# Performance work log

Measured on AMD Instinct MI355X. Metric: run time of the kernel, lower is better.

Reference implementation:

```python
import jax, jax.numpy as jnp
import numpy as np

N_NODES = 100000
N_EDGES = 1600000
N_PAIRS = 200000
IN_C, HID_C, OUT_C = 128, 128, 64


def setup_inputs() -> dict:
    key = jax.random.key(0)
    ks = jax.random.split(key, 10)
    x = jax.random.normal(ks[0], (N_NODES, IN_C), dtype=jnp.float32)
    edge_index = jax.random.randint(ks[1], (2, N_EDGES), 0, N_NODES, dtype=jnp.int64)
    node_i = jax.random.randint(ks[2], (N_PAIRS,), 0, N_NODES, dtype=jnp.int64)
    node_j = jax.random.randint(ks[3], (N_PAIRS,), 0, N_NODES, dtype=jnp.int64)
    def glorot(k, fan_in, fan_out):
        s = jnp.sqrt(6.0 / (fan_in + fan_out))
        return jax.random.uniform(k, (fan_in, fan_out), jnp.float32, -s, s)
    W1 = glorot(ks[4], IN_C, HID_C)
    b1 = jnp.zeros((HID_C,), jnp.float32)
    W2 = glorot(ks[5], HID_C, HID_C)
    b2 = jnp.zeros((HID_C,), jnp.float32)
    W3 = glorot(ks[6], HID_C, OUT_C)
    b3 = jnp.zeros((OUT_C,), jnp.float32)
    return {"x": x, "edge_index": edge_index, "node_i": node_i, "node_j": node_j,
            "W1": W1, "b1": b1, "W2": W2, "b2": b2, "W3": W3, "b3": b3}


def _gcn_layer(h, src, dst, deg_inv, w_e, W, b):
    # h: [N, Cin] -> linear then symmetric-normalized aggregation (with self loops)
    h = h @ W  # [N, Cout]
    msg = h[src] * w_e[:, None]  # [E, Cout] gather + edge weight
    agg = jax.ops.segment_sum(msg, dst, num_segments=N_NODES)
    agg = agg + h * deg_inv[:, None]  # self-loop term: h_i / deg_i
    return agg + b


def reference(x, edge_index, node_i, node_j, W1, b1, W2, b2, W3, b3):
    src, dst = edge_index[0], edge_index[1]
    # GCN normalization with self loops: deg_i = 1 + in-degree
    ones = jnp.ones((N_EDGES,), jnp.float32)
    deg = jax.ops.segment_sum(ones, dst, num_segments=N_NODES) + 1.0
    dinv_sqrt = jax.lax.rsqrt(deg)
    deg_inv = 1.0 / deg
    w_e = dinv_sqrt[src] * dinv_sqrt[dst]  # [E]

    h = _gcn_layer(x, src, dst, deg_inv, w_e, W1, b1)
    h = jax.nn.relu(h)  # dropout is identity in eval mode
    h = _gcn_layer(h, src, dst, deg_inv, w_e, W2, b2)
    h = jax.nn.relu(h)
    h = _gcn_layer(h, src, dst, deg_inv, w_e, W3, b3)

    # dot-product link decode (decode_type=None)
    return jnp.sum(h[node_i] * h[node_j], axis=-1)  # [N_PAIRS]
```

## Files before the change

kernel.cpp:

```cpp
#include <hip/hip_runtime.h>

#define NN 100000
#define NNP 100032
#define NE 1600000
#define NP 200000
#define NBKT 782
#define BCAP 3072
#define BKB 4096

typedef short s16x8 __attribute__((ext_vector_type(8)));
typedef float f32x4 __attribute__((ext_vector_type(4)));

__device__ __forceinline__ unsigned short f2bf(float f) {
  unsigned int u = __float_as_uint(f);
  u += 0x7fffu + ((u >> 16) & 1u);
  return (unsigned short)(u >> 16);
}

__device__ __forceinline__ void upadd(uint u, float& lo, float& hi) {
  lo += __uint_as_float(u << 16);
  hi += __uint_as_float(u & 0xffff0000u);
}

template <int NT>
__device__ __forceinline__ void prepw_dev(const float* __restrict__ W,
                                          uint* __restrict__ Wt, int tid) {
  constexpr int COUT = NT * 16;
  if (tid >= 4 * NT * 64) return;
  int lane = tid & 63, comb = tid >> 6;
  int ks = comb / NT, tl = comb % NT;
  int q = lane >> 4, n = lane & 15;
  uint w[4];
#pragma unroll
  for (int jj = 0; jj < 4; ++jj) {
    int k0 = ks * 32 + q * 8 + 2 * jj;
    uint lo = f2bf(W[k0 * COUT + tl * 16 + n]);
    uint hi = f2bf(W[(k0 + 1) * COUT + tl * 16 + n]);
    w[jj] = lo | (hi << 16);
  }
  ((uint4*)Wt)[comb * 64 + lane] = make_uint4(w[0], w[1], w[2], w[3]);
}

__global__ __launch_bounds__(256) void k_setup(const float* __restrict__ W1,
                                               const float* __restrict__ W2,
                                               const float* __restrict__ W3,
                                               uint* __restrict__ Wt1,
                                               uint* __restrict__ Wt2,
                                               uint* __restrict__ Wt3,
                                               int* __restrict__ gcur) {
  int b = blockIdx.x, t = threadIdx.x;
  if (b < 4) {
    int i = b * 256 + t;
    if (i < 1024) gcur[i] = i * BCAP;
  } else if (b < 12) {
    prepw_dev<8>(W1, Wt1, (b - 4) * 256 + t);
  } else if (b < 20) {
    prepw_dev<8>(W2, Wt2, (b - 12) * 256 + t);
  } else {
    prepw_dev<4>(W3, Wt3, (b - 20) * 256 + t);
  }
}

__global__ __launch_bounds__(256) void k_bucket(const int* __restrict__ ei,
                                                int* __restrict__ gcur,
                                                int* __restrict__ aux) {
  __shared__ int cnt[1024];
  __shared__ int scn[1024];
  __shared__ int cur[1024];
  __shared__ int sc[256];
  __shared__ int sorted[BKB];
  __shared__ unsigned short sbkt[BKB];
  const int t = threadIdx.x;
  const int base = blockIdx.x * BKB;

  for (int i = t; i < 1024; i += 256) cnt[i] = 0;
  __syncthreads();

  int pk[16], bk[16];
#pragma unroll
  for (int i = 0; i < 16; ++i) {
    int e = base + t + 256 * i;
    if (e < NE) {
      int src = ei[e], dst = ei[NE + e];
      bk[i] = dst >> 7;
      pk[i] = src | ((dst & 127) << 17);
      atomicAdd(&cnt[bk[i]], 1);
    } else {
      bk[i] = -1;
    }
  }
  __syncthreads();

  int s0 = cnt[4 * t], s1 = cnt[4 * t + 1], s2 = cnt[4 * t + 2], s3 = cnt[4 * t + 3];
  int local = s0 + s1 + s2 + s3;
  sc[t] = local;
  __syncthreads();
  for (int off = 1; off < 256; off <<= 1) {
    int a = (t >= off) ? sc[t - off] : 0;
    __syncthreads();
    sc[t] += a;
    __syncthreads();
  }
  int b0 = sc[t] - local;
  scn[4 * t] = b0;
  scn[4 * t + 1] = b0 + s0;
  scn[4 * t + 2] = b0 + s0 + s1;
  scn[4 * t + 3] = b0 + s0 + s1 + s2;
  cur[4 * t] = scn[4 * t];
  cur[4 * t + 1] = scn[4 * t + 1];
  cur[4 * t + 2] = scn[4 * t + 2];
  cur[4 * t + 3] = scn[4 * t + 3];
  __syncthreads();
  const int tot = sc[255];

#pragma unroll
  for (int i = 0; i < 16; ++i) {
    if (bk[i] >= 0) {
      int pos = atomicAdd(&cur[bk[i]], 1);
      sorted[pos] = pk[i];
      sbkt[pos] = (unsigned short)bk[i];
    }
  }
  __syncthreads();

  for (int b = t; b < 1024; b += 256) {
    int c = cnt[b];
    if (c > 0) cur[b] = atomicAdd(&gcur[b], c);
  }
  __syncthreads();

  for (int k = t; k < tot; k += 256) {
    int b = sbkt[k];
    aux[cur[b] + (k - scn[b])] = sorted[k];
  }
}

__global__ __launch_bounds__(256) void k_csr(const int* __restrict__ gcur,
                                             const int* __restrict__ aux,
                                             int* __restrict__ row_ptr,
                                             float* __restrict__ dinv,
                                             int* __restrict__ col) {
  __shared__ int red[256];
  __shared__ int c[128];
  __shared__ int cur[128];
  const int b = blockIdx.x, t = threadIdx.x;
  int p = 0;
  for (int i = t; i < b; i += 256) p += gcur[i] - i * BCAP;
  red[t] = p;
  if (t < 128) c[t] = 0;
  __syncthreads();
  for (int off = 128; off > 0; off >>= 1) {
    if (t < off) red[t] += red[t + off];
    __syncthreads();
  }
  const int base = red[0];
  const int m = gcur[b] - b * BCAP;
  const int* a = aux + (size_t)b * BCAP;
  __syncthreads();
  for (int k = t; k < m; k += 256) atomicAdd(&c[a[k] >> 17], 1);
  __syncthreads();
  int val = (t < 128) ? c[t] : 0;
  red[t] = val;
  __syncthreads();
  for (int off = 1; off < 128; off <<= 1) {
    int add = (t >= off && t < 128) ? red[t - off] : 0;
    __syncthreads();
    if (t < 128) red[t] += add;
    __syncthreads();
  }
  if (t < 128) {
    int excl = red[t] - val + base;
    int node = b * 128 + t;
    if (node < NN) {
      row_ptr[node] = excl;
      dinv[node] = rsqrtf((float)(val + 1));
      cur[t] = excl;
    }
  }
  if (b == NBKT - 1 && t == 0) row_ptr[NN] = base + m;
  __syncthreads();
  for (int k = t; k < m; k += 256) {
    int pk2 = a[k];
    int pos = atomicAdd(&cur[pk2 >> 17], 1);
    col[pos] = pk2 & 0x1FFFF;
  }
}

template <int COUT, bool AFP32>
__global__ __launch_bounds__(256) void k_gemm_mfma(const void* __restrict__ Av,
                                                   const uint* __restrict__ Wt,
                                                   const float* __restrict__ dinv,
                                                   unsigned short* __restrict__ T) {
  constexpr int NT = COUT / 16;
  __shared__ __align__(16) uint Wlds[4 * NT * 64 * 4];
  __shared__ __align__(16) unsigned short Obuf[64 * COUT];
  const int t = threadIdx.x;
  {
    const uint4* src = (const uint4*)Wt;
    uint4* dst = (uint4*)Wlds;
    for (int i = t; i < 4 * NT * 64; i += 256) dst[i] = src[i];
  }
  __syncthreads();

  const int wv = t >> 6, lane = t & 63;
  const int n = lane & 15, quad = lane >> 4;
  const int rbase = blockIdx.x * 64 + wv * 16;

  union AB { uint4 u; s16x8 s; };
  AB a[4];
  if constexpr (AFP32) {
    const float* A = (const float*)Av;
    int row = rbase + n;
    if (row >= NN) row = NN - 1;
    const float* ap = A + (size_t)row * 128;
#pragma unroll
    for (int ks = 0; ks < 4; ++ks) {
      float4 v0 = *(const float4*)(ap + ks * 32 + quad * 8);
      float4 v1 = *(const float4*)(ap + ks * 32 + quad * 8 + 4);
      a[ks].u.x = (uint)f2bf(v0.x) | ((uint)f2bf(v0.y) << 16);
      a[ks].u.y = (uint)f2bf(v0.z) | ((uint)f2bf(v0.w) << 16);
      a[ks].u.z = (uint)f2bf(v1.x) | ((uint)f2bf(v1.y) << 16);
      a[ks].u.w = (uint)f2bf(v1.z) | ((uint)f2bf(v1.w) << 16);
    }
  } else {
    const uint4* A = (const uint4*)Av;
    int row = rbase + n;
#pragma unroll
    for (int ks = 0; ks < 4; ++ks) a[ks].u = A[(size_t)row * 16 + ks * 4 + quad];
  }

  f32x4 acc[NT];
#pragma unroll
  for (int tl = 0; tl < NT; ++tl) acc[tl] = (f32x4){0.f, 0.f, 0.f, 0.f};

#pragma unroll
  for (int ks = 0; ks < 4; ++ks) {
#pragma unroll
    for (int tl = 0; tl < NT; ++tl) {
      AB b;
      b.u = *(const uint4*)&Wlds[((ks * NT + tl) * 64 + lane) * 4];
      acc[tl] = __builtin_amdgcn_mfma_f32_16x16x32_bf16(a[ks].s, b.s, acc[tl], 0, 0, 0);
    }
  }

  float4 dv = *(const float4*)(dinv + rbase + quad * 4);
  float dvv[4] = {dv.x, dv.y, dv.z, dv.w};
  unsigned short* ob = Obuf + wv * 16 * COUT;
#pragma unroll
  for (int tl = 0; tl < NT; ++tl)
#pragma unroll
    for (int r = 0; r < 4; ++r)
      ob[(quad * 4 + r) * COUT + tl * 16 + n] = f2bf(acc[tl][r] * dvv[r]);

  uint4* gdst = (uint4*)(T + (size_t)rbase * COUT);
  constexpr int ITER = COUT / 32;
#pragma unroll
  for (int i = 0; i < ITER; ++i) {
    int off16 = i * 64 + lane;
    int lrow = (off16 * 8) / COUT;
    uint4 v = make_uint4(0u, 0u, 0u, 0u);
    if (rbase + lrow < NN) v = *(const uint4*)&ob[off16 * 8];
    gdst[off16] = v;
  }
}

__global__ __launch_bounds__(256) void k_gather12(const int* __restrict__ row_ptr,
                                                  const int* __restrict__ col,
                                                  const uint4* __restrict__ T4,
                                                  const float* __restrict__ dinv,
                                                  const float* __restrict__ bias,
                                                  uint4* __restrict__ An) {
  int w = (blockIdx.x * 256 + threadIdx.x) >> 6;
  int lane = threadIdx.x & 63;
  if (w >= NN) return;
  int s = row_ptr[w], tend = row_ptr[w + 1];
  const int q = lane >> 4;
  const int cl = lane & 15;
  float acc[8] = {0.f, 0.f, 0.f, 0.f, 0.f, 0.f, 0.f, 0.f};
  if (q == 0) {
    uint4 u = T4[(size_t)w * 16 + cl];
    upadd(u.x, acc[0], acc[1]);
    upadd(u.y, acc[2], acc[3]);
    upadd(u.z, acc[4], acc[5]);
    upadd(u.w, acc[6], acc[7]);
  }
  const int iters = (tend - s + 15) >> 4;
  const int m = tend - 1;
  int e = s + q;
  for (int it = 0; it < iters; ++it, e += 16) {
    int i0 = e, i1 = e + 4, i2 = e + 8, i3 = e + 12;
    int c0 = col[min(i0, m)], c1 = col[min(i1, m)];
    int c2 = col[min(i2, m)], c3 = col[min(i3, m)];
    c0 = (i0 < tend) ? c0 : NN;
    c1 = (i1 < tend) ? c1 : NN;
    c2 = (i2 < tend) ? c2 : NN;
    c3 = (i3 < tend) ? c3 : NN;
    uint4 v0 = T4[(size_t)c0 * 16 + cl];
    uint4 v1 = T4[(size_t)c1 * 16 + cl];
    uint4 v2 = T4[(size_t)c2 * 16 + cl];
    uint4 v3 = T4[(size_t)c3 * 16 + cl];
    upadd(v0.x, acc[0], acc[1]); upadd(v0.y, acc[2], acc[3]);
    upadd(v0.z, acc[4], acc[5]); upadd(v0.w, acc[6], acc[7]);
    upadd(v1.x, acc[0], acc[1]); upadd(v1.y, acc[2], acc[3]);
    upadd(v1.z, acc[4], acc[5]); upadd(v1.w, acc[6], acc[7]);
    upadd(v2.x, acc[0], acc[1]); upadd(v2.y, acc[2], acc[3]);
    upadd(v2.z, acc[4], acc[5]); upadd(v2.w, acc[6], acc[7]);
    upadd(v3.x, acc[0], acc[1]); upadd(v3.y, acc[2], acc[3]);
    upadd(v3.z, acc[4], acc[5]); upadd(v3.w, acc[6], acc[7]);
  }
#pragma unroll
  for (int i = 0; i < 8; ++i) {
    acc[i] += __shfl_down(acc[i], 16, 64);
    acc[i] += __shfl_down(acc[i], 32, 64);
  }
  if (q == 0) {
    float4 b0 = *(const float4*)&bias[cl * 8];
    float4 b1 = *(const float4*)&bias[cl * 8 + 4];
    float dv = dinv[w];
    float r[8];
    r[0] = fmaxf(fmaf(dv, acc[0], b0.x), 0.f);
    r[1] = fmaxf(fmaf(dv, acc[1], b0.y), 0.f);
    r[2] = fmaxf(fmaf(dv, acc[2], b0.z), 0.f);
    r[3] = fmaxf(fmaf(dv, acc[3], b0.w), 0.f);
    r[4] = fmaxf(fmaf(dv, acc[4], b1.x), 0.f);
    r[5] = fmaxf(fmaf(dv, acc[5], b1.y), 0.f);
    r[6] = fmaxf(fmaf(dv, acc[6], b1.z), 0.f);
    r[7] = fmaxf(fmaf(dv, acc[7], b1.w), 0.f);
    uint4 o;
    o.x = (uint)f2bf(r[0]) | ((uint)f2bf(r[1]) << 16);
    o.y = (uint)f2bf(r[2]) | ((uint)f2bf(r[3]) << 16);
    o.z = (uint)f2bf(r[4]) | ((uint)f2bf(r[5]) << 16);
    o.w = (uint)f2bf(r[6]) | ((uint)f2bf(r[7]) << 16);
    An[(size_t)w * 16 + cl] = o;
  }
}

__global__ __launch_bounds__(256) void k_gather3(const int* __restrict__ row_ptr,
                                                 const int* __restrict__ col,
                                                 const uint4* __restrict__ T4,
                                                 float* __restrict__ G3) {
  int w = (blockIdx.x * 256 + threadIdx.x) >> 6;
  int lane = threadIdx.x & 63;
  if (w >= NN) return;
  int s = row_ptr[w], tend = row_ptr[w + 1];
  const int g = lane >> 3;
  const int cl = lane & 7;
  float acc[8] = {0.f, 0.f, 0.f, 0.f, 0.f, 0.f, 0.f, 0.f};
  if (g == 0) {
    uint4 u = T4[(size_t)w * 8 + cl];
    upadd(u.x, acc[0], acc[1]);
    upadd(u.y, acc[2], acc[3]);
    upadd(u.z, acc[4], acc[5]);
    upadd(u.w, acc[6], acc[7]);
  }
  const int iters = (tend - s + 15) >> 4;
  const int m = tend - 1;
  int e = s + g;
  for (int it = 0; it < iters; ++it, e += 16) {
    int i0 = e, i1 = e + 8;
    int c0 = col[min(i0, m)], c1 = col[min(i1, m)];
    c0 = (i0 < tend) ? c0 : NN;
    c1 = (i1 < tend) ? c1 : NN;
    uint4 v0 = T4[(size_t)c0 * 8 + cl];
    uint4 v1 = T4[(size_t)c1 * 8 + cl];
    upadd(v0.x, acc[0], acc[1]); upadd(v0.y, acc[2], acc[3]);
    upadd(v0.z, acc[4], acc[5]); upadd(v0.w, acc[6], acc[7]);
    upadd(v1.x, acc[0], acc[1]); upadd(v1.y, acc[2], acc[3]);
    upadd(v1.z, acc[4], acc[5]); upadd(v1.w, acc[6], acc[7]);
  }
#pragma unroll
  for (int i = 0; i < 8; ++i) {
    acc[i] += __shfl_down(acc[i], 8, 64);
    acc[i] += __shfl_down(acc[i], 16, 64);
    acc[i] += __shfl_down(acc[i], 32, 64);
  }
  if (g == 0) {
    float* gp = &G3[(size_t)w * 64 + cl * 8];
    *(float4*)gp = make_float4(acc[0], acc[1], acc[2], acc[3]);
    *(float4*)(gp + 4) = make_float4(acc[4], acc[5], acc[6], acc[7]);
  }
}

__global__ __launch_bounds__(256) void k_decode(const int* __restrict__ ni,
                                                const int* __restrict__ nj,
                                                const float* __restrict__ G3,
                                                const float* __restrict__ dinv,
                                                const float* __restrict__ b3,
                                                float* __restrict__ out) {
  int p = blockIdx.x * 16 + (threadIdx.x >> 4);
  int cl = threadIdx.x & 15;
  int i = ni[p], j = nj[p];
  float4 gi = *(const float4*)&G3[(size_t)i * 64 + cl * 4];
  float4 gj = *(const float4*)&G3[(size_t)j * 64 + cl * 4];
  float4 bb = *(const float4*)&b3[cl * 4];
  float di = dinv[i], dj = dinv[j];
  float v = fmaf(di, gi.x, bb.x) * fmaf(dj, gj.x, bb.x) +
            fmaf(di, gi.y, bb.y) * fmaf(dj, gj.y, bb.y) +
            fmaf(di, gi.z, bb.z) * fmaf(dj, gj.z, bb.z) +
            fmaf(di, gi.w, bb.w) * fmaf(dj, gj.w, bb.w);
  v += __shfl_xor(v, 1, 64);
  v += __shfl_xor(v, 2, 64);
  v += __shfl_xor(v, 4, 64);
  v += __shfl_xor(v, 8, 64);
  if (cl == 0) out[p] = v;
}

extern "C" void kernel_launch(void* const* d_in, const int* in_sizes, int n_in,
                              void* d_out, int out_size, void* d_ws, size_t ws_size,
                              hipStream_t stream) {
  const float* x  = (const float*)d_in[0];
  const int*   ei = (const int*)d_in[1];
  const int*   ni = (const int*)d_in[2];
  const int*   nj = (const int*)d_in[3];
  const float* W1 = (const float*)d_in[4];
  const float* b1 = (const float*)d_in[5];
  const float* W2 = (const float*)d_in[6];
  const float* b2 = (const float*)d_in[7];
  const float* W3 = (const float*)d_in[8];
  const float* b3 = (const float*)d_in[9];
  float* out = (float*)d_out;

  float* dinv    = (float*)d_ws;
  int*   row_ptr = (int*)(dinv + 102400);
  int*   gcur    = row_ptr + 102400;
  int*   col     = gcur + 1024;
  uint*  Wt1     = (uint*)(col + NE);
  uint*  Wt2     = Wt1 + 8192;
  uint*  Wt3     = Wt2 + 8192;
  uint*  Tbf     = Wt3 + 4096;
  uint*  Abf     = Tbf + (size_t)NNP * 64;
  float* G3      = (float*)(Abf + (size_t)NNP * 64);
  int*   aux     = (int*)G3;

  k_setup<<<24, 256, 0, stream>>>(W1, W2, W3, Wt1, Wt2, Wt3, gcur);
  k_bucket<<<(NE + BKB - 1) / BKB, 256, 0, stream>>>(ei, gcur, aux);
  k_csr<<<NBKT, 256, 0, stream>>>(gcur, aux, row_ptr, dinv, col);

  const int GB = NNP / 64;
  const int GATB = (NN * 64 + 255) / 256;

  k_gemm_mfma<128, true><<<GB, 256, 0, stream>>>(x, Wt1, dinv, (unsigned short*)Tbf);
  k_gather12<<<GATB, 256, 0, stream>>>(row_ptr, col, (const uint4*)Tbf, dinv, b1, (uint4*)Abf);
  k_gemm_mfma<128, false><<<GB, 256, 0, stream>>>(Abf, Wt2, dinv, (unsigned short*)Tbf);
  k_gather12<<<GATB, 256, 0, stream>>>(row_ptr, col, (const uint4*)Tbf, dinv, b2, (uint4*)Abf);
  k_gemm_mfma<64, false><<<GB, 256, 0, stream>>>(Abf, Wt3, dinv, (unsigned short*)Tbf);
  k_gather3<<<GATB, 256, 0, stream>>>(row_ptr, col, (const uint4*)Tbf, G3);
  k_decode<<<NP / 16, 256, 0, stream>>>(ni, nj, G3, dinv, b3, out);
}
```

Measured before the change: 345.0 us.

## Split layer-1/2 neighbor gather across eight column slices per node

Rewrites the hidden-layer aggregation so that each node is handled by 8 wavefronts, each covering a 32-byte column slice, instead of one wavefront covering all 128 channels. Each lane now does narrower 8-byte loads, and 16 edge groups per wave process two edges per iteration. The aim is more parallelism and memory-level concurrency, plus a smaller per-block working set of the feature table. The cost is re-reading row_ptr/col 8 times, a longer shuffle reduction, and 8x more wavefronts.

```diff
diff --git a/kernel.cpp b/kernel.cpp
--- a/kernel.cpp
+++ b/kernel.cpp
@@ -266,72 +266,55 @@
 
 __global__ __launch_bounds__(256) void k_gather12(const int* __restrict__ row_ptr,
                                                   const int* __restrict__ col,
-                                                  const uint4* __restrict__ T4,
+                                                  const char* __restrict__ Tb,
                                                   const float* __restrict__ dinv,
                                                   const float* __restrict__ bias,
-                                                  uint4* __restrict__ An) {
-  int w = (blockIdx.x * 256 + threadIdx.x) >> 6;
-  int lane = threadIdx.x & 63;
-  if (w >= NN) return;
-  int s = row_ptr[w], tend = row_ptr[w + 1];
-  const int q = lane >> 4;
-  const int cl = lane & 15;
-  float acc[8] = {0.f, 0.f, 0.f, 0.f, 0.f, 0.f, 0.f, 0.f};
-  if (q == 0) {
-    uint4 u = T4[(size_t)w * 16 + cl];
-    upadd(u.x, acc[0], acc[1]);
-    upadd(u.y, acc[2], acc[3]);
-    upadd(u.z, acc[4], acc[5]);
-    upadd(u.w, acc[6], acc[7]);
-  }
-  const int iters = (tend - s + 15) >> 4;
+                                                  char* __restrict__ Anb) {
+  const int slice = blockIdx.x & 7;
+  const int node = (blockIdx.x >> 3) * 4 + (threadIdx.x >> 6);
+  const int lane = threadIdx.x & 63;
+  const int grp = lane >> 2, cl = lane & 3;
+  const uint soff = (uint)slice * 32 + (uint)cl * 8;
+  int s = row_ptr[node], tend = row_ptr[node + 1];
+  float a0 = 0.f, a1 = 0.f, a2 = 0.f, a3 = 0.f;
+  if (grp == 0) {
+    uint2 u = *(const uint2*)(Tb + (uint)node * 256 + soff);
+    upadd(u.x, a0, a1);
+    upadd(u.y, a2, a3);
+  }
+  const int iters = (tend - s + 31) >> 5;
   const int m = tend - 1;
-  int e = s + q;
-  for (int it = 0; it < iters; ++it, e += 16) {
-    int i0 = e, i1 = e + 4, i2 = e + 8, i3 = e + 12;
+  int e = s + grp;
+  for (int it = 0; it < iters; ++it, e += 32) {
+    int i0 = e, i1 = e + 16;
     int c0 = col[min(i0, m)], c1 = col[min(i1, m)];
-    int c2 = col[min(i2, m)], c3 = col[min(i3, m)];
     c0 = (i0 < tend) ? c0 : NN;
     c1 = (i1 < tend) ? c1 : NN;
-    c2 = (i2 < tend) ? c2 : NN;
-    c3 = (i3 < tend) ? c3 : NN;
-    uint4 v0 = T4[(size_t)c0 * 16 + cl];
-    uint4 v1 = T4[(size_t)c1 * 16 + cl];
-    uint4 v2 = T4[(size_t)c2 * 16 + cl];
-    uint4 v3 = T4[(size_t)c3 * 16 + cl];
-    upadd(v0.x, acc[0], acc[1]); upadd(v0.y, acc[2], acc[3]);
-    upadd(v0.z, acc[4], acc[5]); upadd(v0.w, acc[6], acc[7]);
-    upadd(v1.x, acc[0], acc[1]); upadd(v1.y, acc[2], acc[3]);
-    upadd(v1.z, acc[4], acc[5]); upadd(v1.w, acc[6], acc[7]);
-    upadd(v2.x, acc[0], acc[1]); upadd(v2.y, acc[2], acc[3]);
-    upadd(v2.z, acc[4], acc[5]); upadd(v2.w, acc[6], acc[7]);
-    upadd(v3.x, acc[0], acc[1]); upadd(v3.y, acc[2], acc[3]);
-    upadd(v3.z, acc[4], acc[5]); upadd(v3.w, acc[6], acc[7]);
-  }
-#pragma unroll
-  for (int i = 0; i < 8; ++i) {
-    acc[i] += __shfl_down(acc[i], 16, 64);
-    acc[i] += __shfl_down(acc[i], 32, 64);
-  }
-  if (q == 0) {
-    float4 b0 = *(const float4*)&bias[cl * 8];
-    float4 b1 = *(const float4*)&bias[cl * 8 + 4];
-    float dv = dinv[w];
-    float r[8];
-    r[0] = fmaxf(fmaf(dv, acc[0], b0.x), 0.f);
-    r[1] = fmaxf(fmaf(dv, acc[1], b0.y), 0.f);
-    r[2] = fmaxf(fmaf(dv, acc[2], b0.z), 0.f);
-    r[3] = fmaxf(fmaf(dv, acc[3], b0.w), 0.f);
-    r[4] = fmaxf(fmaf(dv, acc[4], b1.x), 0.f);
-    r[5] = fmaxf(fmaf(dv, acc[5], b1.y), 0.f);
-    r[6] = fmaxf(fmaf(dv, acc[6], b1.z), 0.f);
-    r[7] = fmaxf(fmaf(dv, acc[7], b1.w), 0.f);
-    uint4 o;
-    o.x = (uint)f2bf(r[0]) | ((uint)f2bf(r[1]) << 16);
-    o.y = (uint)f2bf(r[2]) | ((uint)f2bf(r[3]) << 16);
-    o.z = (uint)f2bf(r[4]) | ((uint)f2bf(r[5]) << 16);
-    o.w = (uint)f2bf(r[6]) | ((uint)f2bf(r[7]) << 16);
-    An[(size_t)w * 16 + cl] = o;
+    uint2 v0 = *(const uint2*)(Tb + (uint)c0 * 256 + soff);
+    uint2 v1 = *(const uint2*)(Tb + (uint)c1 * 256 + soff);
+    upadd(v0.x, a0, a1);
+    upadd(v0.y, a2, a3);
+    upadd(v1.x, a0, a1);
+    upadd(v1.y, a2, a3);
+  }
+#pragma unroll
+  for (int off = 4; off < 64; off <<= 1) {
+    a0 += __shfl_down(a0, off, 64);
+    a1 += __shfl_down(a1, off, 64);
+    a2 += __shfl_down(a2, off, 64);
+    a3 += __shfl_down(a3, off, 64);
+  }
+  if (lane < 4) {
+    float4 bb = *(const float4*)&bias[slice * 16 + cl * 4];
+    float dv = dinv[node];
+    float r0 = fmaxf(fmaf(dv, a0, bb.x), 0.f);
+    float r1 = fmaxf(fmaf(dv, a1, bb.y), 0.f);
+    float r2 = fmaxf(fmaf(dv, a2, bb.z), 0.f);
+    float r3 = fmaxf(fmaf(dv, a3, bb.w), 0.f);
+    uint2 o;
+    o.x = (uint)f2bf(r0) | ((uint)f2bf(r1) << 16);
+    o.y = (uint)f2bf(r2) | ((uint)f2bf(r3) << 16);
+    *(uint2*)(Anb + (uint)node * 256 + soff) = o;
   }
 }
 
@@ -437,12 +420,13 @@
   k_csr<<<NBKT, 256, 0, stream>>>(gcur, aux, row_ptr, dinv, col);
 
   const int GB = NNP / 64;
+  const int G12B = (NN / 4) * 8;
   const int GATB = (NN * 64 + 255) / 256;
 
   k_gemm_mfma<128, true><<<GB, 256, 0, stream>>>(x, Wt1, dinv, (unsigned short*)Tbf);
-  k_gather12<<<GATB, 256, 0, stream>>>(row_ptr, col, (const uint4*)Tbf, dinv, b1, (uint4*)Abf);
+  k_gather12<<<G12B, 256, 0, stream>>>(row_ptr, col, (const char*)Tbf, dinv, b1, (char*)Abf);
   k_gemm_mfma<128, false><<<GB, 256, 0, stream>>>(Abf, Wt2, dinv, (unsigned short*)Tbf);
-  k_gather12<<<GATB, 256, 0, stream>>>(row_ptr, col, (const uint4*)Tbf, dinv, b2, (uint4*)Abf);
+  k_gather12<<<G12B, 256, 0, stream>>>(row_ptr, col, (const char*)Tbf, dinv, b2, (char*)Abf);
   k_gemm_mfma<64, false><<<GB, 256, 0, stream>>>(Abf, Wt3, dinv, (unsigned short*)Tbf);
   k_gather3<<<GATB, 256, 0, stream>>>(row_ptr, col, (const uint4*)Tbf, G3);
   k_decode<<<NP / 16, 256, 0, stream>>>(ni, nj, G3, dinv, b3, out);
```

Result: slower. 695.7 us (+101.7%).

## Split layer-1/2 gather into two column halves with separate block ranges

Applied to the files above, without the earlier changes.

The 128-channel gather is split into two launches' worth of blocks, each handling 64 channels (128 bytes) of every node, with 8 lanes per half-row and 8 edge groups per wave. The first half of the grid processes channels 0-63 for all nodes and the second half processes channels 64-127. This shrinks the working set touched in the feature table at any one time so it fits the cache better. In exchange, the row_ptr and col indices are read twice and each thread keeps fewer loads in flight per iteration. Offsets now use 32-bit arithmetic.

```diff
diff --git a/kernel.cpp b/kernel.cpp
--- a/kernel.cpp
+++ b/kernel.cpp
@@ -7,6 +7,7 @@
 #define NBKT 782
 #define BCAP 3072
 #define BKB 4096
+#define G12H 25000
 
 typedef short s16x8 __attribute__((ext_vector_type(8)));
 typedef float f32x4 __attribute__((ext_vector_type(4)));
@@ -266,19 +267,20 @@
 
 __global__ __launch_bounds__(256) void k_gather12(const int* __restrict__ row_ptr,
                                                   const int* __restrict__ col,
-                                                  const uint4* __restrict__ T4,
+                                                  const char* __restrict__ Tb,
                                                   const float* __restrict__ dinv,
                                                   const float* __restrict__ bias,
-                                                  uint4* __restrict__ An) {
-  int w = (blockIdx.x * 256 + threadIdx.x) >> 6;
-  int lane = threadIdx.x & 63;
-  if (w >= NN) return;
-  int s = row_ptr[w], tend = row_ptr[w + 1];
-  const int q = lane >> 4;
-  const int cl = lane & 15;
+                                                  char* __restrict__ Anb) {
+  const int half = (blockIdx.x >= G12H) ? 1 : 0;
+  const int node = (blockIdx.x - half * G12H) * 4 + (threadIdx.x >> 6);
+  const int lane = threadIdx.x & 63;
+  const int g = lane >> 3;
+  const int cl = lane & 7;
+  const uint hoff = (uint)half * 128 + (uint)cl * 16;
+  int s = row_ptr[node], tend = row_ptr[node + 1];
   float acc[8] = {0.f, 0.f, 0.f, 0.f, 0.f, 0.f, 0.f, 0.f};
-  if (q == 0) {
-    uint4 u = T4[(size_t)w * 16 + cl];
+  if (g == 0) {
+    uint4 u = *(const uint4*)(Tb + (uint)node * 256 + hoff);
     upadd(u.x, acc[0], acc[1]);
     upadd(u.y, acc[2], acc[3]);
     upadd(u.z, acc[4], acc[5]);
@@ -286,37 +288,30 @@
   }
   const int iters = (tend - s + 15) >> 4;
   const int m = tend - 1;
-  int e = s + q;
+  int e = s + g;
   for (int it = 0; it < iters; ++it, e += 16) {
-    int i0 = e, i1 = e + 4, i2 = e + 8, i3 = e + 12;
+    int i0 = e, i1 = e + 8;
     int c0 = col[min(i0, m)], c1 = col[min(i1, m)];
-    int c2 = col[min(i2, m)], c3 = col[min(i3, m)];
     c0 = (i0 < tend) ? c0 : NN;
     c1 = (i1 < tend) ? c1 : NN;
-    c2 = (i2 < tend) ? c2 : NN;
-    c3 = (i3 < tend) ? c3 : NN;
-    uint4 v0 = T4[(size_t)c0 * 16 + cl];
-    uint4 v1 = T4[(size_t)c1 * 16 + cl];
-    uint4 v2 = T4[(size_t)c2 * 16 + cl];
-    uint4 v3 = T4[(size_t)c3 * 16 + cl];
+    uint4 v0 = *(const uint4*)(Tb + (uint)c0 * 256 + hoff);
+    uint4 v1 = *(const uint4*)(Tb + (uint)c1 * 256 + hoff);
     upadd(v0.x, acc[0], acc[1]); upadd(v0.y, acc[2], acc[3]);
     upadd(v0.z, acc[4], acc[5]); upadd(v0.w, acc[6], acc[7]);
     upadd(v1.x, acc[0], acc[1]); upadd(v1.y, acc[2], acc[3]);
     upadd(v1.z, acc[4], acc[5]); upadd(v1.w, acc[6], acc[7]);
-    upadd(v2.x, acc[0], acc[1]); upadd(v2.y, acc[2], acc[3]);
-    upadd(v2.z, acc[4], acc[5]); upadd(v2.w, acc[6], acc[7]);
-    upadd(v3.x, acc[0], acc[1]); upadd(v3.y, acc[2], acc[3]);
-    upadd(v3.z, acc[4], acc[5]); upadd(v3.w, acc[6], acc[7]);
   }
 #pragma unroll
   for (int i = 0; i < 8; ++i) {
+    acc[i] += __shfl_down(acc[i], 8, 64);
     acc[i] += __shfl_down(acc[i], 16, 64);
     acc[i] += __shfl_down(acc[i], 32, 64);
   }
-  if (q == 0) {
-    float4 b0 = *(const float4*)&bias[cl * 8];
-    float4 b1 = *(const float4*)&bias[cl * 8 + 4];
-    float dv = dinv[w];
+  if (g == 0) {
+    const float* bp = bias + half * 64 + cl * 8;
+    float4 b0 = *(const float4*)bp;
+    float4 b1 = *(const float4*)(bp + 4);
+    float dv = dinv[node];
     float r[8];
     r[0] = fmaxf(fmaf(dv, acc[0], b0.x), 0.f);
     r[1] = fmaxf(fmaf(dv, acc[1], b0.y), 0.f);
@@ -331,7 +326,7 @@
     o.y = (uint)f2bf(r[2]) | ((uint)f2bf(r[3]) << 16);
     o.z = (uint)f2bf(r[4]) | ((uint)f2bf(r[5]) << 16);
     o.w = (uint)f2bf(r[6]) | ((uint)f2bf(r[7]) << 16);
-    An[(size_t)w * 16 + cl] = o;
+    *(uint4*)(Anb + (uint)node * 256 + hoff) = o;
   }
 }
 
@@ -440,9 +435,9 @@
   const int GATB = (NN * 64 + 255) / 256;
 
   k_gemm_mfma<128, true><<<GB, 256, 0, stream>>>(x, Wt1, dinv, (unsigned short*)Tbf);
-  k_gather12<<<GATB, 256, 0, stream>>>(row_ptr, col, (const uint4*)Tbf, dinv, b1, (uint4*)Abf);
+  k_gather12<<<2 * G12H, 256, 0, stream>>>(row_ptr, col, (const char*)Tbf, dinv, b1, (char*)Abf);
   k_gemm_mfma<128, false><<<GB, 256, 0, stream>>>(Abf, Wt2, dinv, (unsigned short*)Tbf);
-  k_gather12<<<GATB, 256, 0, stream>>>(row_ptr, col, (const uint4*)Tbf, dinv, b2, (uint4*)Abf);
+  k_gather12<<<2 * G12H, 256, 0, stream>>>(row_ptr, col, (const char*)Tbf, dinv, b2, (char*)Abf);
   k_gemm_mfma<64, false><<<GB, 256, 0, stream>>>(Abf, Wt3, dinv, (unsigned short*)Tbf);
   k_gather3<<<GATB, 256, 0, stream>>>(row_ptr, col, (const uint4*)Tbf, G3);
   k_decode<<<NP / 16, 256, 0, stream>>>(ni, nj, G3, dinv, b3, out);
```

After: 379.9 us. +10.1%, slower.

## Fuse layer gather-aggregation with next layer's MFMA GEMM per 16-node block

Applied to the files above, without the earlier changes.

Replaces the separate gather kernel and following GEMM kernel for layers 2 and 3 with one kernel. Each block aggregates 16 nodes into LDS, then runs the bf16 MFMA with the next weight matrix and writes the transformed features directly. This removes two kernel launches and the round trip of the intermediate activation buffer through global memory. In exchange, every 16-node block reloads the full weight matrix into LDS, and the gather loop is serialized as four nodes per wave.

```diff
diff --git a/kernel.cpp b/kernel.cpp
--- a/kernel.cpp
+++ b/kernel.cpp
@@ -186,12 +186,11 @@
   }
 }
 
-template <int COUT, bool AFP32>
-__global__ __launch_bounds__(256) void k_gemm_mfma(const void* __restrict__ Av,
-                                                   const uint* __restrict__ Wt,
-                                                   const float* __restrict__ dinv,
-                                                   unsigned short* __restrict__ T) {
-  constexpr int NT = COUT / 16;
+__global__ __launch_bounds__(256) void k_gemm1(const float* __restrict__ A,
+                                               const uint* __restrict__ Wt,
+                                               const float* __restrict__ dinv,
+                                               unsigned short* __restrict__ T) {
+  constexpr int NT = 8, COUT = 128;
   __shared__ __align__(16) uint Wlds[4 * NT * 64 * 4];
   __shared__ __align__(16) unsigned short Obuf[64 * COUT];
   const int t = threadIdx.x;
@@ -208,8 +207,7 @@
 
   union AB { uint4 u; s16x8 s; };
   AB a[4];
-  if constexpr (AFP32) {
-    const float* A = (const float*)Av;
+  {
     int row = rbase + n;
     if (row >= NN) row = NN - 1;
     const float* ap = A + (size_t)row * 128;
@@ -222,11 +220,6 @@
       a[ks].u.z = (uint)f2bf(v1.x) | ((uint)f2bf(v1.y) << 16);
       a[ks].u.w = (uint)f2bf(v1.z) | ((uint)f2bf(v1.w) << 16);
     }
-  } else {
-    const uint4* A = (const uint4*)Av;
-    int row = rbase + n;
-#pragma unroll
-    for (int ks = 0; ks < 4; ++ks) a[ks].u = A[(size_t)row * 16 + ks * 4 + quad];
   }
 
   f32x4 acc[NT];
@@ -253,9 +246,8 @@
       ob[(quad * 4 + r) * COUT + tl * 16 + n] = f2bf(acc[tl][r] * dvv[r]);
 
   uint4* gdst = (uint4*)(T + (size_t)rbase * COUT);
-  constexpr int ITER = COUT / 32;
-#pragma unroll
-  for (int i = 0; i < ITER; ++i) {
+#pragma unroll
+  for (int i = 0; i < 4; ++i) {
     int off16 = i * 64 + lane;
     int lrow = (off16 * 8) / COUT;
     uint4 v = make_uint4(0u, 0u, 0u, 0u);
@@ -264,74 +256,139 @@
   }
 }
 
-__global__ __launch_bounds__(256) void k_gather12(const int* __restrict__ row_ptr,
-                                                  const int* __restrict__ col,
-                                                  const uint4* __restrict__ T4,
-                                                  const float* __restrict__ dinv,
-                                                  const float* __restrict__ bias,
-                                                  uint4* __restrict__ An) {
-  int w = (blockIdx.x * 256 + threadIdx.x) >> 6;
-  int lane = threadIdx.x & 63;
-  if (w >= NN) return;
-  int s = row_ptr[w], tend = row_ptr[w + 1];
-  const int q = lane >> 4;
-  const int cl = lane & 15;
-  float acc[8] = {0.f, 0.f, 0.f, 0.f, 0.f, 0.f, 0.f, 0.f};
-  if (q == 0) {
-    uint4 u = T4[(size_t)w * 16 + cl];
-    upadd(u.x, acc[0], acc[1]);
-    upadd(u.y, acc[2], acc[3]);
-    upadd(u.z, acc[4], acc[5]);
-    upadd(u.w, acc[6], acc[7]);
-  }
-  const int iters = (tend - s + 15) >> 4;
-  const int m = tend - 1;
-  int e = s + q;
-  for (int it = 0; it < iters; ++it, e += 16) {
-    int i0 = e, i1 = e + 4, i2 = e + 8, i3 = e + 12;
-    int c0 = col[min(i0, m)], c1 = col[min(i1, m)];
-    int c2 = col[min(i2, m)], c3 = col[min(i3, m)];
-    c0 = (i0 < tend) ? c0 : NN;
-    c1 = (i1 < tend) ? c1 : NN;
-    c2 = (i2 < tend) ? c2 : NN;
-    c3 = (i3 < tend) ? c3 : NN;
-    uint4 v0 = T4[(size_t)c0 * 16 + cl];
-    uint4 v1 = T4[(size_t)c1 * 16 + cl];
-    uint4 v2 = T4[(size_t)c2 * 16 + cl];
-    uint4 v3 = T4[(size_t)c3 * 16 + cl];
-    upadd(v0.x, acc[0], acc[1]); upadd(v0.y, acc[2], acc[3]);
-    upadd(v0.z, acc[4], acc[5]); upadd(v0.w, acc[6], acc[7]);
-    upadd(v1.x, acc[0], acc[1]); upadd(v1.y, acc[2], acc[3]);
-    upadd(v1.z, acc[4], acc[5]); upadd(v1.w, acc[6], acc[7]);
-    upadd(v2.x, acc[0], acc[1]); upadd(v2.y, acc[2], acc[3]);
-    upadd(v2.z, acc[4], acc[5]); upadd(v2.w, acc[6], acc[7]);
-    upadd(v3.x, acc[0], acc[1]); upadd(v3.y, acc[2], acc[3]);
-    upadd(v3.z, acc[4], acc[5]); upadd(v3.w, acc[6], acc[7]);
-  }
-#pragma unroll
-  for (int i = 0; i < 8; ++i) {
-    acc[i] += __shfl_down(acc[i], 16, 64);
-    acc[i] += __shfl_down(acc[i], 32, 64);
-  }
-  if (q == 0) {
-    float4 b0 = *(const float4*)&bias[cl * 8];
-    float4 b1 = *(const float4*)&bias[cl * 8 + 4];
-    float dv = dinv[w];
-    float r[8];
-    r[0] = fmaxf(fmaf(dv, acc[0], b0.x), 0.f);
-    r[1] = fmaxf(fmaf(dv, acc[1], b0.y), 0.f);
-    r[2] = fmaxf(fmaf(dv, acc[2], b0.z), 0.f);
-    r[3] = fmaxf(fmaf(dv, acc[3], b0.w), 0.f);
-    r[4] = fmaxf(fmaf(dv, acc[4], b1.x), 0.f);
-    r[5] = fmaxf(fmaf(dv, acc[5], b1.y), 0.f);
-    r[6] = fmaxf(fmaf(dv, acc[6], b1.z), 0.f);
-    r[7] = fmaxf(fmaf(dv, acc[7], b1.w), 0.f);
-    uint4 o;
-    o.x = (uint)f2bf(r[0]) | ((uint)f2bf(r[1]) << 16);
-    o.y = (uint)f2bf(r[2]) | ((uint)f2bf(r[3]) << 16);
-    o.z = (uint)f2bf(r[4]) | ((uint)f2bf(r[5]) << 16);
-    o.w = (uint)f2bf(r[6]) | ((uint)f2bf(r[7]) << 16);
-    An[(size_t)w * 16 + cl] = o;
+template <int COUT>
+__global__ __launch_bounds__(256) void k_gagemm(const int* __restrict__ row_ptr,
+                                                const int* __restrict__ col,
+                                                const char* __restrict__ Tin,
+                                                const float* __restrict__ dinv,
+                                                const float* __restrict__ bias,
+                                                const uint* __restrict__ Wt,
+                                                unsigned short* __restrict__ Tout) {
+  constexpr int NT = COUT / 16;
+  constexpr int TLW = NT / 4;
+  constexpr int OSTR = COUT + 8;
+  __shared__ __align__(16) uint Wlds[4 * NT * 64 * 4];
+  __shared__ __align__(16) uint4 Alds[16 * 17];
+  __shared__ __align__(16) unsigned short Obuf[16 * OSTR];
+  const int t = threadIdx.x;
+  {
+    const uint4* src = (const uint4*)Wt;
+    uint4* dst = (uint4*)Wlds;
+    for (int i = t; i < 4 * NT * 64; i += 256) dst[i] = src[i];
+  }
+
+  const int wv = t >> 6, lane = t & 63;
+  const int nbase = blockIdx.x * 16;
+  const int q = lane >> 4, cl = lane & 15;
+
+#pragma unroll 1
+  for (int i = 0; i < 4; ++i) {
+    const int node = nbase + wv * 4 + i;
+    int s = 0, tend = 0;
+    if (node < NN) { s = row_ptr[node]; tend = row_ptr[node + 1]; }
+    float acc[8] = {0.f, 0.f, 0.f, 0.f, 0.f, 0.f, 0.f, 0.f};
+    if (q == 0) {
+      uint4 u = *(const uint4*)(Tin + (uint)node * 256 + cl * 16);
+      upadd(u.x, acc[0], acc[1]);
+      upadd(u.y, acc[2], acc[3]);
+      upadd(u.z, acc[4], acc[5]);
+      upadd(u.w, acc[6], acc[7]);
+    }
+    const int iters = (tend - s + 15) >> 4;
+    const int m = tend - 1;
+    int e = s + q;
+    for (int it = 0; it < iters; ++it, e += 16) {
+      int i0 = e, i1 = e + 4, i2 = e + 8, i3 = e + 12;
+      int c0 = col[min(i0, m)], c1 = col[min(i1, m)];
+      int c2 = col[min(i2, m)], c3 = col[min(i3, m)];
+      c0 = (i0 < tend) ? c0 : NN;
+      c1 = (i1 < tend) ? c1 : NN;
+      c2 = (i2 < tend) ? c2 : NN;
+      c3 = (i3 < tend) ? c3 : NN;
+      uint4 v0 = *(const uint4*)(Tin + (uint)c0 * 256 + cl * 16);
+      uint4 v1 = *(const uint4*)(Tin + (uint)c1 * 256 + cl * 16);
+      uint4 v2 = *(const uint4*)(Tin + (uint)c2 * 256 + cl * 16);
+      uint4 v3 = *(const uint4*)(Tin + (uint)c3 * 256 + cl * 16);
+      upadd(v0.x, acc[0], acc[1]); upadd(v0.y, acc[2], acc[3]);
+      upadd(v0.z, acc[4], acc[5]); upadd(v0.w, acc[6], acc[7]);
+      upadd(v1.x, acc[0], acc[1]); upadd(v1.y, acc[2], acc[3]);
+      upadd(v1.z, acc[4], acc[5]); upadd(v1.w, acc[6], acc[7]);
+      upadd(v2.x, acc[0], acc[1]); upadd(v2.y, acc[2], acc[3]);
+      upadd(v2.z, acc[4], acc[5]); upadd(v2.w, acc[6], acc[7]);
+      upadd(v3.x, acc[0], acc[1]); upadd(v3.y, acc[2], acc[3]);
+      upadd(v3.z, acc[4], acc[5]); upadd(v3.w, acc[6], acc[7]);
+    }
+#pragma unroll
+    for (int k = 0; k < 8; ++k) {
+      acc[k] += __shfl_down(acc[k], 16, 64);
+      acc[k] += __shfl_down(acc[k], 32, 64);
+    }
+    if (q == 0) {
+      float4 b0 = *(const float4*)&bias[cl * 8];
+      float4 b1 = *(const float4*)&bias[cl * 8 + 4];
+      float dv = dinv[node];
+      float r[8];
+      r[0] = fmaxf(fmaf(dv, acc[0], b0.x), 0.f);
+      r[1] = fmaxf(fmaf(dv, acc[1], b0.y), 0.f);
+      r[2] = fmaxf(fmaf(dv, acc[2], b0.z), 0.f);
+      r[3] = fmaxf(fmaf(dv, acc[3], b0.w), 0.f);
+      r[4] = fmaxf(fmaf(dv, acc[4], b1.x), 0.f);
+      r[5] = fmaxf(fmaf(dv, acc[5], b1.y), 0.f);
+      r[6] = fmaxf(fmaf(dv, acc[6], b1.z), 0.f);
+      r[7] = fmaxf(fmaf(dv, acc[7], b1.w), 0.f);
+      uint4 o;
+      o.x = (uint)f2bf(r[0]) | ((uint)f2bf(r[1]) << 16);
+      o.y = (uint)f2bf(r[2]) | ((uint)f2bf(r[3]) << 16);
+      o.z = (uint)f2bf(r[4]) | ((uint)f2bf(r[5]) << 16);
+      o.w = (uint)f2bf(r[6]) | ((uint)f2bf(r[7]) << 16);
+      Alds[(wv * 4 + i) * 17 + cl] = o;
+    }
+  }
+  __syncthreads();
+
+  const int n = lane & 15, quad = lane >> 4;
+  union AB { uint4 u; s16x8 s; };
+  f32x4 acc2[TLW];
+#pragma unroll
+  for (int j = 0; j < TLW; ++j) acc2[j] = (f32x4){0.f, 0.f, 0.f, 0.f};
+#pragma unroll
+  for (int ks = 0; ks < 4; ++ks) {
+    AB a;
+    a.u = Alds[n * 17 + ks * 4 + quad];
+#pragma unroll
+    for (int j = 0; j < TLW; ++j) {
+      int tl = wv * TLW + j;
+      AB b;
+      b.u = *(const uint4*)&Wlds[((ks * NT + tl) * 64 + lane) * 4];
+      acc2[j] = __builtin_amdgcn_mfma_f32_16x16x32_bf16(a.s, b.s, acc2[j], 0, 0, 0);
+    }
+  }
+
+  float4 dv4 = *(const float4*)(dinv + nbase + quad * 4);
+  float dvv[4] = {dv4.x, dv4.y, dv4.z, dv4.w};
+#pragma unroll
+  for (int j = 0; j < TLW; ++j) {
+    int tl = wv * TLW + j;
+#pragma unroll
+    for (int r = 0; r < 4; ++r)
+      Obuf[(quad * 4 + r) * OSTR + tl * 16 + n] = f2bf(acc2[j][r] * dvv[r]);
+  }
+  __syncthreads();
+
+  if constexpr (COUT == 128) {
+    int lrow = lane >> 4 | (wv << 2);
+    int row = t >> 4, c16 = t & 15;
+    uint4 v = make_uint4(0u, 0u, 0u, 0u);
+    if (nbase + row < NN) v = *(const uint4*)&Obuf[row * OSTR + c16 * 8];
+    ((uint4*)(Tout + (size_t)nbase * COUT))[row * 16 + c16] = v;
+    (void)lrow;
+  } else {
+    if (t < 128) {
+      int row = t >> 3, c16 = t & 7;
+      uint4 v = make_uint4(0u, 0u, 0u, 0u);
+      if (nbase + row < NN) v = *(const uint4*)&Obuf[row * OSTR + c16 * 8];
+      ((uint4*)(Tout + (size_t)nbase * COUT))[row * 8 + c16] = v;
+    }
   }
 }
 
@@ -428,8 +485,8 @@
   uint*  Wt2     = Wt1 + 8192;
   uint*  Wt3     = Wt2 + 8192;
   uint*  Tbf     = Wt3 + 4096;
-  uint*  Abf     = Tbf + (size_t)NNP * 64;
-  float* G3      = (float*)(Abf + (size_t)NNP * 64);
+  uint*  T2      = Tbf + (size_t)NNP * 64;
+  float* G3      = (float*)(T2 + (size_t)NNP * 64);
   int*   aux     = (int*)G3;
 
   k_setup<<<24, 256, 0, stream>>>(W1, W2, W3, Wt1, Wt2, Wt3, gcur);
@@ -437,13 +494,14 @@
   k_csr<<<NBKT, 256, 0, stream>>>(gcur, aux, row_ptr, dinv, col);
 
   const int GB = NNP / 64;
+  const int FB = NNP / 16;
   const int GATB = (NN * 64 + 255) / 256;
 
-  k_gemm_mfma<128, true><<<GB, 256, 0, stream>>>(x, Wt1, dinv, (unsigned short*)Tbf);
-  k_gather12<<<GATB, 256, 0, stream>>>(row_ptr, col, (const uint4*)Tbf, dinv, b1, (uint4*)Abf);
-  k_gemm_mfma<128, false><<<GB, 256, 0, stream>>>(Abf, Wt2, dinv, (unsigned short*)Tbf);
-  k_gather12<<<GATB, 256, 0, stream>>>(row_ptr, col, (const uint4*)Tbf, dinv, b2, (uint4*)Abf);
-  k_gemm_mfma<64, false><<<GB, 256, 0, stream>>>(Abf, Wt3, dinv, (unsigned short*)Tbf);
+  k_gemm1<<<GB, 256, 0, stream>>>(x, Wt1, dinv, (unsigned short*)Tbf);
+  k_gagemm<128><<<FB, 256, 0, stream>>>(row_ptr, col, (const char*)Tbf, dinv, b1,
+                                        Wt2, (unsigned short*)T2);
+  k_gagemm<64><<<FB, 256, 0, stream>>>(row_ptr, col, (const char*)T2, dinv, b2,
+                                       Wt3, (unsigned short*)Tbf);
   k_gather3<<<GATB, 256, 0, stream>>>(row_ptr, col, (const uint4*)Tbf, G3);
   k_decode<<<NP / 16, 256, 0, stream>>>(ni, nj, G3, dinv, b3, out);
 }
```

Result: slower. 364.8 us (+5.7%).
